# Performance work log

Hardware: AMD Instinct MI355X
Metric: run time of the kernel (lower is better)

## Reference

```python
import jax, jax.numpy as jnp
import numpy as np

N, T, H, W, C = 4, 8, 64, 64, 512
WS = 8  # window size; H, W are exact multiples so pad/depad are identity


def setup_inputs() -> dict:
    key = jax.random.key(0)
    k1, k2, k3, k4 = jax.random.split(key, 4)
    x = jax.random.normal(k1, (N, T, H, W, C), dtype=jnp.float32)
    local_pos_embed = jax.random.normal(k2, (WS, WS, C), dtype=jnp.float32)
    W_in = jax.random.normal(k3, (3 * C, C), dtype=jnp.float32) * 0.02
    b_in = jnp.zeros((3 * C,), dtype=jnp.float32)
    W_out = jax.random.normal(k4, (C, C), dtype=jnp.float32) * 0.02
    b_out = jnp.zeros((C,), dtype=jnp.float32)
    return {"x": x, "local_pos_embed": local_pos_embed, "W_in": W_in,
            "b_in": b_in, "W_out": W_out, "b_out": b_out, "num_heads": 8}


def reference(x, local_pos_embed, W_in, b_in, W_out, b_out, num_heads):
    n, t, h, w, c = x.shape
    ws = local_pos_embed.shape[0]
    nh, nw = h // ws, w // ws
    head_dim = c // num_heads
    scale = 1.0 / jnp.sqrt(jnp.asarray(head_dim, dtype=x.dtype))

    # window partition: (N*T, H, W, C) -> (N*T*nh*nw, ws*ws, C)
    xw = x.reshape(n * t, nh, ws, nw, ws, c)
    xw = xw.transpose(0, 1, 3, 2, 4, 5).reshape(n * t * nh * nw, ws * ws, c)

    pos = local_pos_embed.reshape(ws * ws, c)  # flatten(0,1)
    qk_in = xw + pos[None, :, :]               # pos added to q,k only

    Wq, Wk, Wv = W_in[:c], W_in[c:2 * c], W_in[2 * c:]
    bq, bk, bv = b_in[:c], b_in[c:2 * c], b_in[2 * c:]

    B, S = qk_in.shape[0], qk_in.shape[1]
    q = (qk_in @ Wq.T + bq).reshape(B, S, num_heads, head_dim)
    k = (qk_in @ Wk.T + bk).reshape(B, S, num_heads, head_dim)
    v = (xw @ Wv.T + bv).reshape(B, S, num_heads, head_dim)

    scores = jnp.einsum('bqhd,bkhd->bhqk', q * scale, k)
    attn = jax.nn.softmax(scores, axis=-1)
    out = jnp.einsum('bhqk,bkhd->bqhd', attn, v).reshape(B, S, c)
    out = out @ W_out.T + b_out

    # reverse window partition
    out = out.reshape(n * t, nh, nw, ws, ws, c)
    out = out.transpose(0, 1, 3, 2, 4, 5).reshape(n, t, h, w, c)
    return out
```

## Files before the change

kernel.cpp:

```cpp
#include <hip/hip_runtime.h>

typedef _Float16 f16;
typedef unsigned int u32;
typedef f16 f16x8 __attribute__((ext_vector_type(8)));
typedef f16 f16x4 __attribute__((ext_vector_type(4)));
typedef float f32x4 __attribute__((ext_vector_type(4)));


__device__ __forceinline__ int src_row(int m) {
    int win = m >> 6, s = m & 63;
    return ((win >> 6) << 12) | (((win >> 3) & 7) << 9) | ((s >> 3) << 6) |
           ((win & 7) << 3) | (s & 7);
}

__device__ __forceinline__ void gload_lds16(const void* g, void* lds) {
    __builtin_amdgcn_global_load_lds(
        (const __attribute__((address_space(1))) u32*)g,
        (__attribute__((address_space(3))) u32*)lds, 16, 0, 0);
}

__device__ __forceinline__ f16* sp(char* S, int r, int c) {
    return (f16*)(S + r * 1024 + ((c * 2) ^ ((r & 7) << 4)));
}

__global__ __launch_bounds__(256) void prep_weights_k(
        const float* __restrict__ Wi, const float* __restrict__ Wo,
        f16* __restrict__ Wi_h, f16* __restrict__ Wo_h) {
    int i = blockIdx.x * 256 + threadIdx.x;
    const float4* src;
    f16* dst;
    int idx;
    if (i < 196608) { src = (const float4*)Wi; dst = Wi_h; idx = i; }
    else            { src = (const float4*)Wo; dst = Wo_h; idx = i - 196608; }
    float4 v = src[idx];
    f16x4 h = {(f16)v.x, (f16)v.y, (f16)v.z, (f16)v.w};
    *(f16x4*)(dst + (size_t)idx * 4) = h;
}

__global__ __launch_bounds__(256) void prep_bias_k(
        const float* __restrict__ pos, const float* __restrict__ Wi,
        const float* __restrict__ b_in, float* __restrict__ biasT) {
    int idx = blockIdx.x * 256 + threadIdx.x;
    int s = idx / 1536, o = idx % 1536;
    float acc = b_in[o];
    if (o < 1024) {
        const float4* p4 = (const float4*)(pos + (size_t)s * 512);
        const float4* w4 = (const float4*)(Wi + (size_t)o * 512);
        #pragma unroll 4
        for (int c = 0; c < 128; ++c) {
            float4 a = p4[c], b = w4[c];
            acc += a.x * b.x + a.y * b.y + a.z * b.z + a.w * b.w;
        }
    }
    biasT[idx] = acc;
}

__global__ __launch_bounds__(256) void prep_x_k(
        const float* __restrict__ x, f16* __restrict__ xh, int m0) {
    int i = blockIdx.x * 256 + threadIdx.x;
    int ml = i >> 6, c8 = (i & 63) * 8;
    int sr = src_row(m0 + ml);
    const float4* s4 = (const float4*)(x + (size_t)sr * 512 + c8);
    float4 a = s4[0], b = s4[1];
    f16x8 hv = {(f16)a.x, (f16)a.y, (f16)a.z, (f16)a.w,
                (f16)b.x, (f16)b.y, (f16)b.z, (f16)b.w};
    *(f16x8*)(xh + (size_t)ml * 512 + c8) = hv;
}

__global__ void __launch_bounds__(512, 2) qkv_gemm8_k(
        const f16* __restrict__ xh, const f16* __restrict__ Wh,
        const float* __restrict__ biasT, f16* __restrict__ qkv, int nblk) {
    extern __shared__ f16 lds[];
    int tid = threadIdx.x;
    int lane = tid & 63, wid = tid >> 6;
    int l15 = lane & 15, g = lane >> 4;
    int wm = wid >> 2, wn = wid & 3;
    int sid = (blockIdx.x & 7) * (nblk >> 3) + (blockIdx.x >> 3);
    int bm = sid / 6, bn = sid % 6;
    const f16* Ap = xh + (size_t)bm * 256 * 512;
    const f16* Bp = Wh + (size_t)bn * 256 * 512;

    int li0 = tid, li1 = tid + 512;
    int r0 = li0 >> 3, c0 = li0 & 7, r1 = li1 >> 3, c1 = li1 & 7;
    int off0 = r0 * 512 + ((c0 ^ (r0 & 7)) * 8);
    int off1 = r1 * 512 + ((c1 ^ (r1 & 7)) * 8);

    auto stage = [&](const f16* panel, int ldsbase, int tt, int h) {
        int tb = tt & 1;
        int dst = ldsbase + (tb * 2 + h) * 8192 + wid * 512;
        const f16* src = panel + h * 65536 + tt * 64;
        gload_lds16(src + off0, (void*)&lds[dst]);
        gload_lds16(src + off1, (void*)&lds[dst + 4096]);
    };

    f32x4 acc[8][4];
    f32x4 zero4 = {0.f, 0.f, 0.f, 0.f};
    #pragma unroll
    for (int a = 0; a < 8; ++a)
        #pragma unroll
        for (int b = 0; b < 4; ++b) acc[a][b] = zero4;
    f16x8 bf[4][2];

    stage(Ap, 0, 0, 0); stage(Ap, 0, 0, 1);
    stage(Bp, 32768, 0, 0); stage(Bp, 32768, 0, 1);
    stage(Ap, 0, 1, 0); stage(Ap, 0, 1, 1);
    stage(Bp, 32768, 1, 0); stage(Bp, 32768, 1, 1);
    asm volatile("s_waitcnt vmcnt(0)" ::: "memory");
    __builtin_amdgcn_s_barrier();

    #pragma unroll
    for (int tt = 0; tt < 8; ++tt) {
        int tb = tt & 1;
        const f16* Ab = &lds[(tb * 2 + wm) * 8192];
        const f16* Bb = &lds[32768 + (tb * 2 + (wn >> 1)) * 8192];
        #pragma unroll
        for (int q = 0; q < 4; ++q) {
            f16x8 af[2][2];
            #pragma unroll
            for (int ml = 0; ml < 2; ++ml) {
                int rr = (q * 2 + ml) * 16 + l15;
                #pragma unroll
                for (int ks = 0; ks < 2; ++ks)
                    af[ml][ks] = *(const f16x8*)&Ab[rr * 64 + (((ks * 4 + g) ^ (rr & 7)) * 8)];
            }
            if (q == 0) {
                #pragma unroll
                for (int nf = 0; nf < 4; ++nf) {
                    int rb = (wn & 1) * 64 + nf * 16 + l15;
                    #pragma unroll
                    for (int ks = 0; ks < 2; ++ks)
                        bf[nf][ks] = *(const f16x8*)&Bb[rb * 64 + (((ks * 4 + g) ^ (rb & 7)) * 8)];
                }
            }
            if (q <= 1) {
                if ((tt & 1) ? (tt + 1 < 8) : (tt >= 2)) stage(Ap, 0, tt + 1, q);
            } else {
                if (tt + 2 < 8) stage(Bp, 32768, tt + 2, q - 2);
            }
            __builtin_amdgcn_s_barrier();
            __builtin_amdgcn_s_setprio(1);
            #pragma unroll
            for (int ml = 0; ml < 2; ++ml)
                #pragma unroll
                for (int nf = 0; nf < 4; ++nf)
                    #pragma unroll
                    for (int ks = 0; ks < 2; ++ks)
                        acc[q * 2 + ml][nf] = __builtin_amdgcn_mfma_f32_16x16x32_f16(
                            af[ml][ks], bf[nf][ks], acc[q * 2 + ml][nf], 0, 0, 0);
            __builtin_amdgcn_s_setprio(0);
            if (q == 3) {
                if (tt < 6)       asm volatile("s_waitcnt vmcnt(4)" ::: "memory");
                else if (tt == 6) asm volatile("s_waitcnt vmcnt(0)" ::: "memory");
            }
            __builtin_amdgcn_s_barrier();
        }
    }

    int browg = bm * 256 + wm * 128, bcolg = bn * 256 + wn * 64;
    #pragma unroll
    for (int mf = 0; mf < 8; ++mf) {
        #pragma unroll
        for (int nf = 0; nf < 4; ++nf) {
            int col = bcolg + nf * 16 + l15;
            #pragma unroll
            for (int j = 0; j < 4; ++j) {
                int row = browg + mf * 16 + g * 4 + j;
                float v = acc[mf][nf][j] + biasT[(row & 63) * 1536 + col];
                qkv[(size_t)row * 1536 + col] = (f16)v;
            }
        }
    }
}

__global__ __launch_bounds__(512) void attn_out_k(
        const f16* __restrict__ qkv, const f16* __restrict__ Woh,
        const float* __restrict__ b_out, float* __restrict__ out, int w0) {
    __shared__ __align__(16) char S[64 * 1024];
    int tid = threadIdx.x;
    int lane = tid & 63, h = tid >> 6;
    int l15 = lane & 15, g = lane >> 4;
    const f16* base = qkv + (size_t)blockIdx.x * 64 * 1536;
    int qc = h * 64, kc = 512 + h * 64, vc = 1024 + h * 64;

    f32x4 zero4 = {0.f, 0.f, 0.f, 0.f};
    f32x4 acc[4][4];
    #pragma unroll
    for (int a = 0; a < 4; ++a)
        #pragma unroll
        for (int b = 0; b < 4; ++b) acc[a][b] = zero4;

    {
        f16x8 qf[4][2], kf[4][2];
        #pragma unroll
        for (int mf = 0; mf < 4; ++mf)
            #pragma unroll
            for (int ks = 0; ks < 2; ++ks)
                qf[mf][ks] = *reinterpret_cast<const f16x8*>(base + (size_t)(mf * 16 + l15) * 1536 + qc + ks * 32 + g * 8);
        #pragma unroll
        for (int nf = 0; nf < 4; ++nf)
            #pragma unroll
            for (int ks = 0; ks < 2; ++ks)
                kf[nf][ks] = *reinterpret_cast<const f16x8*>(base + (size_t)(nf * 16 + l15) * 1536 + kc + ks * 32 + g * 8);
        #pragma unroll
        for (int ks = 0; ks < 2; ++ks)
            #pragma unroll
            for (int mf = 0; mf < 4; ++mf)
                #pragma unroll
                for (int nf = 0; nf < 4; ++nf)
                    acc[mf][nf] = __builtin_amdgcn_mfma_f32_16x16x32_f16(qf[mf][ks], kf[nf][ks], acc[mf][nf], 0, 0, 0);
    }

    f16x8 vf[4][2];
    #pragma unroll
    for (int nf = 0; nf < 4; ++nf)
        #pragma unroll
        for (int ks = 0; ks < 2; ++ks) {
            f16x8 v;
            #pragma unroll
            for (int j = 0; j < 8; ++j)
                v[j] = base[(size_t)(ks * 32 + g * 8 + j) * 1536 + vc + nf * 16 + l15];
            vf[nf][ks] = v;
        }

    #pragma unroll
    for (int mf = 0; mf < 4; ++mf) {
        #pragma unroll
        for (int j = 0; j < 4; ++j) {
            float mx = -1e30f;
            #pragma unroll
            for (int nf = 0; nf < 4; ++nf) mx = fmaxf(mx, acc[mf][nf][j]);
            #pragma unroll
            for (int off = 1; off < 16; off <<= 1) mx = fmaxf(mx, __shfl_xor(mx, off));
            float e[4], sum = 0.f;
            #pragma unroll
            for (int nf = 0; nf < 4; ++nf) {
                e[nf] = __expf((acc[mf][nf][j] - mx) * 0.125f);
                sum += e[nf];
            }
            #pragma unroll
            for (int off = 1; off < 16; off <<= 1) sum += __shfl_xor(sum, off);
            float rinv = __fdividef(1.0f, sum);
            int row = mf * 16 + g * 4 + j;
            #pragma unroll
            for (int nf = 0; nf < 4; ++nf)
                *sp(S, row, h * 64 + nf * 16 + l15) = (f16)(e[nf] * rinv);
        }
    }

    f32x4 acc2[4][4];
    #pragma unroll
    for (int a = 0; a < 4; ++a)
        #pragma unroll
        for (int b = 0; b < 4; ++b) acc2[a][b] = zero4;
    #pragma unroll
    for (int ks = 0; ks < 2; ++ks)
        #pragma unroll
        for (int mf = 0; mf < 4; ++mf) {
            f16x8 pa = *reinterpret_cast<const f16x8*>(sp(S, mf * 16 + l15, h * 64 + ks * 32 + g * 8));
            #pragma unroll
            for (int nf = 0; nf < 4; ++nf)
                acc2[mf][nf] = __builtin_amdgcn_mfma_f32_16x16x32_f16(pa, vf[nf][ks], acc2[mf][nf], 0, 0, 0);
        }
    #pragma unroll
    for (int mf = 0; mf < 4; ++mf)
        #pragma unroll
        for (int nf = 0; nf < 4; ++nf)
            #pragma unroll
            for (int j = 0; j < 4; ++j)
                *sp(S, mf * 16 + g * 4 + j, h * 64 + nf * 16 + l15) = (f16)acc2[mf][nf][j];

    __syncthreads();

    int ocol0 = h * 64;
    float bo[4];
    #pragma unroll
    for (int nf = 0; nf < 4; ++nf) bo[nf] = b_out[ocol0 + nf * 16 + l15];

    #pragma unroll
    for (int a = 0; a < 4; ++a)
        #pragma unroll
        for (int b = 0; b < 4; ++b) acc[a][b] = zero4;
    for (int ks = 0; ks < 16; ++ks) {
        f16x8 af[4], bf[4];
        #pragma unroll
        for (int mf = 0; mf < 4; ++mf)
            af[mf] = *reinterpret_cast<const f16x8*>(sp(S, mf * 16 + l15, ks * 32 + g * 8));
        #pragma unroll
        for (int nf = 0; nf < 4; ++nf)
            bf[nf] = *reinterpret_cast<const f16x8*>(Woh + (size_t)(ocol0 + nf * 16 + l15) * 512 + ks * 32 + g * 8);
        #pragma unroll
        for (int mf = 0; mf < 4; ++mf)
            #pragma unroll
            for (int nf = 0; nf < 4; ++nf)
                acc[mf][nf] = __builtin_amdgcn_mfma_f32_16x16x32_f16(af[mf], bf[nf], acc[mf][nf], 0, 0, 0);
    }

    int wglob = w0 + blockIdx.x;
    #pragma unroll
    for (int mf = 0; mf < 4; ++mf) {
        #pragma unroll
        for (int j = 0; j < 4; ++j) {
            int srow = src_row(wglob * 64 + mf * 16 + g * 4 + j);
            #pragma unroll
            for (int nf = 0; nf < 4; ++nf)
                out[(size_t)srow * 512 + ocol0 + nf * 16 + l15] = acc[mf][nf][j] + bo[nf];
        }
    }
}

extern "C" void kernel_launch(void* const* d_in, const int* in_sizes, int n_in,
                              void* d_out, int out_size, void* d_ws, size_t ws_size,
                              hipStream_t stream) {
    (void)in_sizes; (void)n_in; (void)out_size;
    const float* x     = (const float*)d_in[0];
    const float* pos   = (const float*)d_in[1];
    const float* W_in  = (const float*)d_in[2];
    const float* b_in  = (const float*)d_in[3];
    const float* W_out = (const float*)d_in[4];
    const float* b_out = (const float*)d_in[5];
    float* out = (float*)d_out;

    char* ws = (char*)d_ws;
    f16*   Wi_h  = (f16*)ws;
    f16*   Wo_h  = (f16*)(ws + 1572864);
    float* biasT = (float*)(ws + 2097152);
    const size_t fixed = 2490368;

    int chunks = 4;
    while (chunks < 64) {
        size_t need = fixed + ((size_t)131072 / chunks) * 4096;
        if (need <= ws_size) break;
        chunks <<= 1;
    }
    int Mc = 131072 / chunks;
    f16* xh  = (f16*)(ws + fixed);
    f16* qkv = (f16*)(ws + fixed + (size_t)Mc * 1024);
    int nblk = (Mc / 256) * 6;

    static_cast<void>(hipFuncSetAttribute((const void*)qkv_gemm8_k,
        hipFuncAttributeMaxDynamicSharedMemorySize, 131072));

    prep_weights_k<<<1024, 256, 0, stream>>>(W_in, W_out, Wi_h, Wo_h);
    prep_bias_k<<<384, 256, 0, stream>>>(pos, W_in, b_in, biasT);
    for (int c = 0; c < chunks; ++c) {
        int m0 = c * Mc;
        prep_x_k<<<Mc / 4, 256, 0, stream>>>(x, xh, m0);
        qkv_gemm8_k<<<nblk, 512, 131072, stream>>>(xh, Wi_h, biasT, qkv, nblk);
        attn_out_k<<<Mc / 64, 512, 0, stream>>>(qkv, Wo_h, b_out, out, c * (Mc / 64));
    }
}
```

Baseline: 650.0 us.

## Split attention and output projection into separate kernels with tiled LDS-pipelined GEMM

Output projection moves out of the fused attention kernel, which re-read W_out from global memory per 64-row window, into a 256x256-tiled GEMM. That GEMM stages A/B panels into LDS with async global-to-LDS loads, double-buffers them, and remaps blocks for better grid locality. Attention now writes its per-head results to a global fp16 buffer that reuses the xh workspace. The default chunk count is lowered to 1 so that fewer, larger launches occur when workspace allows. This adds a global round trip for the attention output and an extra launch per chunk.

After: 635.0 us. -2.3%, faster.

```diff
diff --git a/kernel.cpp b/kernel.cpp
--- a/kernel.cpp
+++ b/kernel.cpp
@@ -172,9 +172,8 @@
     }
 }
 
-__global__ __launch_bounds__(512) void attn_out_k(
-        const f16* __restrict__ qkv, const f16* __restrict__ Woh,
-        const float* __restrict__ b_out, float* __restrict__ out, int w0) {
+__global__ __launch_bounds__(512) void attn_k(
+        const f16* __restrict__ qkv, f16* __restrict__ attn_h) {
     __shared__ __align__(16) char S[64 * 1024];
     int tid = threadIdx.x;
     int lane = tid & 63, h = tid >> 6;
@@ -222,6 +221,7 @@
             vf[nf][ks] = v;
         }
 
+    char* Sh = S + h * 8192;
     #pragma unroll
     for (int mf = 0; mf < 4; ++mf) {
         #pragma unroll
@@ -243,7 +243,7 @@
             int row = mf * 16 + g * 4 + j;
             #pragma unroll
             for (int nf = 0; nf < 4; ++nf)
-                *sp(S, row, h * 64 + nf * 16 + l15) = (f16)(e[nf] * rinv);
+                *(f16*)(Sh + row * 128 + (((nf * 16 + l15) * 2) ^ ((row & 7) << 4))) = (f16)(e[nf] * rinv);
         }
     }
 
@@ -256,54 +256,124 @@
     for (int ks = 0; ks < 2; ++ks)
         #pragma unroll
         for (int mf = 0; mf < 4; ++mf) {
-            f16x8 pa = *reinterpret_cast<const f16x8*>(sp(S, mf * 16 + l15, h * 64 + ks * 32 + g * 8));
+            int rr = mf * 16 + l15;
+            f16x8 pa = *reinterpret_cast<const f16x8*>(Sh + rr * 128 + (((ks * 32 + g * 8) * 2) ^ ((rr & 7) << 4)));
             #pragma unroll
             for (int nf = 0; nf < 4; ++nf)
                 acc2[mf][nf] = __builtin_amdgcn_mfma_f32_16x16x32_f16(pa, vf[nf][ks], acc2[mf][nf], 0, 0, 0);
         }
+
+    f16* dst = attn_h + (size_t)blockIdx.x * 64 * 512 + h * 64;
     #pragma unroll
     for (int mf = 0; mf < 4; ++mf)
         #pragma unroll
         for (int nf = 0; nf < 4; ++nf)
             #pragma unroll
             for (int j = 0; j < 4; ++j)
-                *sp(S, mf * 16 + g * 4 + j, h * 64 + nf * 16 + l15) = (f16)acc2[mf][nf][j];
-
-    __syncthreads();
-
-    int ocol0 = h * 64;
-    float bo[4];
-    #pragma unroll
-    for (int nf = 0; nf < 4; ++nf) bo[nf] = b_out[ocol0 + nf * 16 + l15];
-
-    #pragma unroll
-    for (int a = 0; a < 4; ++a)
+                dst[(size_t)(mf * 16 + g * 4 + j) * 512 + nf * 16 + l15] = (f16)acc2[mf][nf][j];
+}
+
+__global__ void __launch_bounds__(512, 2) proj_gemm8_k(
+        const f16* __restrict__ attn_h, const f16* __restrict__ Woh,
+        const float* __restrict__ b_out, float* __restrict__ out, int nblk, int m0) {
+    extern __shared__ f16 lds[];
+    int tid = threadIdx.x;
+    int lane = tid & 63, wid = tid >> 6;
+    int l15 = lane & 15, g = lane >> 4;
+    int wm = wid >> 2, wn = wid & 3;
+    int sid = (blockIdx.x & 7) * (nblk >> 3) + (blockIdx.x >> 3);
+    int bm = sid >> 1, bn = sid & 1;
+    const f16* Ap = attn_h + (size_t)bm * 256 * 512;
+    const f16* Bp = Woh + (size_t)bn * 256 * 512;
+
+    int li0 = tid, li1 = tid + 512;
+    int r0 = li0 >> 3, c0 = li0 & 7, r1 = li1 >> 3, c1 = li1 & 7;
+    int off0 = r0 * 512 + ((c0 ^ (r0 & 7)) * 8);
+    int off1 = r1 * 512 + ((c1 ^ (r1 & 7)) * 8);
+
+    auto stage = [&](const f16* panel, int ldsbase, int tt, int h) {
+        int tb = tt & 1;
+        int dst = ldsbase + (tb * 2 + h) * 8192 + wid * 512;
+        const f16* src = panel + h * 65536 + tt * 64;
+        gload_lds16(src + off0, (void*)&lds[dst]);
+        gload_lds16(src + off1, (void*)&lds[dst + 4096]);
+    };
+
+    f32x4 acc[8][4];
+    f32x4 zero4 = {0.f, 0.f, 0.f, 0.f};
+    #pragma unroll
+    for (int a = 0; a < 8; ++a)
         #pragma unroll
         for (int b = 0; b < 4; ++b) acc[a][b] = zero4;
-    for (int ks = 0; ks < 16; ++ks) {
-        f16x8 af[4], bf[4];
-        #pragma unroll
-        for (int mf = 0; mf < 4; ++mf)
-            af[mf] = *reinterpret_cast<const f16x8*>(sp(S, mf * 16 + l15, ks * 32 + g * 8));
-        #pragma unroll
-        for (int nf = 0; nf < 4; ++nf)
-            bf[nf] = *reinterpret_cast<const f16x8*>(Woh + (size_t)(ocol0 + nf * 16 + l15) * 512 + ks * 32 + g * 8);
-        #pragma unroll
-        for (int mf = 0; mf < 4; ++mf)
-            #pragma unroll
-            for (int nf = 0; nf < 4; ++nf)
-                acc[mf][nf] = __builtin_amdgcn_mfma_f32_16x16x32_f16(af[mf], bf[nf], acc[mf][nf], 0, 0, 0);
-    }
-
-    int wglob = w0 + blockIdx.x;
-    #pragma unroll
-    for (int mf = 0; mf < 4; ++mf) {
-        #pragma unroll
-        for (int j = 0; j < 4; ++j) {
-            int srow = src_row(wglob * 64 + mf * 16 + g * 4 + j);
-            #pragma unroll
-            for (int nf = 0; nf < 4; ++nf)
-                out[(size_t)srow * 512 + ocol0 + nf * 16 + l15] = acc[mf][nf][j] + bo[nf];
+    f16x8 bf[4][2];
+
+    stage(Ap, 0, 0, 0); stage(Ap, 0, 0, 1);
+    stage(Bp, 32768, 0, 0); stage(Bp, 32768, 0, 1);
+    stage(Ap, 0, 1, 0); stage(Ap, 0, 1, 1);
+    stage(Bp, 32768, 1, 0); stage(Bp, 32768, 1, 1);
+    asm volatile("s_waitcnt vmcnt(0)" ::: "memory");
+    __builtin_amdgcn_s_barrier();
+
+    #pragma unroll
+    for (int tt = 0; tt < 8; ++tt) {
+        int tb = tt & 1;
+        const f16* Ab = &lds[(tb * 2 + wm) * 8192];
+        const f16* Bb = &lds[32768 + (tb * 2 + (wn >> 1)) * 8192];
+        #pragma unroll
+        for (int q = 0; q < 4; ++q) {
+            f16x8 af[2][2];
+            #pragma unroll
+            for (int ml = 0; ml < 2; ++ml) {
+                int rr = (q * 2 + ml) * 16 + l15;
+                #pragma unroll
+                for (int ks = 0; ks < 2; ++ks)
+                    af[ml][ks] = *(const f16x8*)&Ab[rr * 64 + (((ks * 4 + g) ^ (rr & 7)) * 8)];
+            }
+            if (q == 0) {
+                #pragma unroll
+                for (int nf = 0; nf < 4; ++nf) {
+                    int rb = (wn & 1) * 64 + nf * 16 + l15;
+                    #pragma unroll
+                    for (int ks = 0; ks < 2; ++ks)
+                        bf[nf][ks] = *(const f16x8*)&Bb[rb * 64 + (((ks * 4 + g) ^ (rb & 7)) * 8)];
+                }
+            }
+            if (q <= 1) {
+                if ((tt & 1) ? (tt + 1 < 8) : (tt >= 2)) stage(Ap, 0, tt + 1, q);
+            } else {
+                if (tt + 2 < 8) stage(Bp, 32768, tt + 2, q - 2);
+            }
+            __builtin_amdgcn_s_barrier();
+            __builtin_amdgcn_s_setprio(1);
+            #pragma unroll
+            for (int ml = 0; ml < 2; ++ml)
+                #pragma unroll
+                for (int nf = 0; nf < 4; ++nf)
+                    #pragma unroll
+                    for (int ks = 0; ks < 2; ++ks)
+                        acc[q * 2 + ml][nf] = __builtin_amdgcn_mfma_f32_16x16x32_f16(
+                            af[ml][ks], bf[nf][ks], acc[q * 2 + ml][nf], 0, 0, 0);
+            __builtin_amdgcn_s_setprio(0);
+            if (q == 3) {
+                if (tt < 6)       asm volatile("s_waitcnt vmcnt(4)" ::: "memory");
+                else if (tt == 6) asm volatile("s_waitcnt vmcnt(0)" ::: "memory");
+            }
+            __builtin_amdgcn_s_barrier();
+        }
+    }
+
+    int browg = bm * 256 + wm * 128, bcolg = bn * 256 + wn * 64;
+    #pragma unroll
+    for (int nf = 0; nf < 4; ++nf) {
+        int col = bcolg + nf * 16 + l15;
+        float bo = b_out[col];
+        #pragma unroll
+        for (int mf = 0; mf < 8; ++mf) {
+            #pragma unroll
+            for (int j = 0; j < 4; ++j) {
+                int srow = src_row(m0 + browg + mf * 16 + g * 4 + j);
+                out[(size_t)srow * 512 + col] = acc[mf][nf][j] + bo;
+            }
         }
     }
 }
@@ -326,7 +396,7 @@
     float* biasT = (float*)(ws + 2097152);
     const size_t fixed = 2490368;
 
-    int chunks = 4;
+    int chunks = 1;
     while (chunks < 64) {
         size_t need = fixed + ((size_t)131072 / chunks) * 4096;
         if (need <= ws_size) break;
@@ -335,9 +405,12 @@
     int Mc = 131072 / chunks;
     f16* xh  = (f16*)(ws + fixed);
     f16* qkv = (f16*)(ws + fixed + (size_t)Mc * 1024);
-    int nblk = (Mc / 256) * 6;
+    int nblk  = (Mc / 256) * 6;
+    int nblk2 = (Mc / 256) * 2;
 
     static_cast<void>(hipFuncSetAttribute((const void*)qkv_gemm8_k,
+        hipFuncAttributeMaxDynamicSharedMemorySize, 131072));
+    static_cast<void>(hipFuncSetAttribute((const void*)proj_gemm8_k,
         hipFuncAttributeMaxDynamicSharedMemorySize, 131072));
 
     prep_weights_k<<<1024, 256, 0, stream>>>(W_in, W_out, Wi_h, Wo_h);
@@ -346,6 +419,7 @@
         int m0 = c * Mc;
         prep_x_k<<<Mc / 4, 256, 0, stream>>>(x, xh, m0);
         qkv_gemm8_k<<<nblk, 512, 131072, stream>>>(xh, Wi_h, biasT, qkv, nblk);
-        attn_out_k<<<Mc / 64, 512, 0, stream>>>(qkv, Wo_h, b_out, out, c * (Mc / 64));
-    }
-}
+        attn_k<<<Mc / 64, 512, 0, stream>>>(qkv, xh);
+        proj_gemm8_k<<<nblk2, 512, 131072, stream>>>(xh, Wo_h, b_out, out, nblk2, m0);
+    }
+}
```
